# Optimization experiments

Hardware: AMD Instinct MI355X
Metric: run time of the kernel (lower is better)

## Reference

```python
import jax, jax.numpy as jnp
import numpy as np

B, S, T = 2, 4096, 4096
SRC, DST, WIDTH = 512, 512, 128
BLK = 128  # JAKAL_ADDITIVE_ROUTE_BLOCK_SIZE default


def setup_inputs() -> dict:
    key = jax.random.key(0)
    ks = jax.random.split(key, 7)
    return {
        "source_val": jax.random.normal(ks[0], (B, S, SRC), jnp.float32),
        "target_val": jax.random.normal(ks[1], (B, T, DST), jnp.float32),
        "Ws": jax.random.normal(ks[2], (WIDTH, SRC), jnp.float32) * 0.02,  # source_proj weight
        "Wt": jax.random.normal(ks[3], (WIDTH, DST), jnp.float32) * 0.02,  # target_proj weight
        "ws_out": jax.random.normal(ks[4], (WIDTH,), jnp.float32) * 0.02,  # source_out weight
        "wt_out": jax.random.normal(ks[5], (WIDTH,), jnp.float32) * 0.02,  # target_out weight
        "w_int": jax.random.normal(ks[6], (WIDTH,), jnp.float32) * 0.02,   # interaction_weight
        "bias": jnp.zeros((), jnp.float32),
    }


def reference(source_val, target_val, Ws, Wt, ws_out, wt_out, w_int, bias):
    # Projections (Linear without bias): y = x @ W.T
    ps = jnp.einsum('bsd,wd->bsw', source_val, Ws)   # [B,S,WIDTH]
    pt = jnp.einsum('btd,wd->btw', target_val, Wt)   # [B,T,WIDTH]
    s_lin = jnp.einsum('bsw,w->bs', ps, ws_out)      # [B,S]
    t_lin = jnp.einsum('btw,w->bt', pt, wt_out)      # [B,T]

    nblk = S // BLK
    # Block the source axis, matching the torch block loop (avoids a [B,S,T,W] tensor).
    ps_blocks = ps.reshape(B, nblk, BLK, WIDTH).transpose(1, 0, 2, 3)   # [nblk,B,BLK,W]
    sl_blocks = s_lin.reshape(B, nblk, BLK).transpose(1, 0, 2)          # [nblk,B,BLK]

    def block_scores(_, xs):
        ps_blk, sl_blk = xs
        # SiLU of the elementwise bilinear interaction, then low-rank weighted reduce.
        inter = jax.nn.silu(ps_blk[:, :, None, :] * pt[:, None, :, :])  # [B,BLK,T,W]
        sc = jnp.einsum('bktw,w->bkt', inter, w_int)
        sc = sc + sl_blk[:, :, None] + t_lin[:, None, :] + bias
        return None, sc

    _, out = jax.lax.scan(block_scores, None, (ps_blocks, sl_blocks))   # [nblk,B,BLK,T]
    return out.transpose(1, 0, 2, 3).reshape(B, S, T)
```

## Files before the change

kernel.cpp:

```cpp
#include <hip/hip_runtime.h>
#include <cstdint>
#include <cstddef>

#define B_ 2
#define S_ 4096
#define T_ 4096
#define D_ 512
#define W_ 128

#define A0C (-0.0006958f)
#define A1C (0.2529946f)
#define A2C (-0.0226345f)
#define A3C (0.0022173f)
#define A4C (-0.00011668f)
#define ZCUT 2.5f
#define ROWCAP 65536

typedef __attribute__((ext_vector_type(8))) short bf16x8;
typedef __attribute__((ext_vector_type(4))) float f32x4;

__device__ __forceinline__ uint16_t f2bf(float f){
  uint32_t u = __float_as_uint(f);
  u += 0x7FFFu + ((u >> 16) & 1u);
  return (uint16_t)(u >> 16);
}
__device__ __forceinline__ float bf2f(uint16_t h){
  return __uint_as_float(((uint32_t)h) << 16);
}

__device__ __forceinline__ void gl_lds16(const void* g, void* l){
  __builtin_amdgcn_global_load_lds(
      (const __attribute__((address_space(1))) void*)g,
      (__attribute__((address_space(3))) void*)l, 16, 0, 0);
}

union F4 { float4 v; float f[4]; };

template<int INBF>
__global__ void prep_k(const void* __restrict__ Ws, const void* __restrict__ Wt,
                       const void* __restrict__ wso, const void* __restrict__ wto,
                       const void* __restrict__ wi, const void* __restrict__ bias,
                       float* __restrict__ WsT, float* __restrict__ WtT,
                       float* __restrict__ wsof, float* __restrict__ wtof,
                       float* __restrict__ wif, float* __restrict__ cbias,
                       float* __restrict__ maxT, int* __restrict__ rowCnt){
  auto cv = [](const void* p, int i)->float{
    if (INBF) return bf2f(((const uint16_t*)p)[i]);
    return ((const float*)p)[i];
  };
  const void* in = (blockIdx.x & 1) ? Wt : Ws;
  float* out = (blockIdx.x & 1) ? WtT : WsT;
  int base = (blockIdx.x >> 1) * 4096;
  for (int o = base + threadIdx.x; o < base + 4096; o += blockDim.x){
    int d = o >> 7, w = o & (W_ - 1);
    out[o] = cv(in, w * D_ + d);
  }
  if (blockIdx.x == 1){
    maxT[threadIdx.x] = 0.f;
  }
  if (blockIdx.x == 0){
    if (threadIdx.x < W_){
      wsof[threadIdx.x] = cv(wso, threadIdx.x);
      wtof[threadIdx.x] = cv(wto, threadIdx.x);
      wif[threadIdx.x]  = cv(wi,  threadIdx.x);
    }
    __syncthreads();
    if (threadIdx.x == 0){
      float s = 0.f;
      for (int k = 0; k < W_; ++k) s += wif[k];
      cbias[0] = cv(bias, 0) + A0C * s;
      rowCnt[0] = 0;
    }
  }
}

template<int INBF, int MODE>
__global__ __launch_bounds__(256) void proj_k(const void* __restrict__ xraw,
        const float* __restrict__ WT, const float* __restrict__ wout,
        const float* __restrict__ wint,
        float* __restrict__ pT, float* __restrict__ lin,
        uint16_t* __restrict__ feat, float* __restrict__ maxT){
  __shared__ float xl[64 * 18];
  __shared__ float wl[64 * 128];
  int tid = threadIdx.x;
  int tx = tid & 31, ty = tid >> 5;
  int rowBase = blockIdx.x * 16;
  float acc[2][4] = {};
  for (int c = 0; c < 8; ++c){
    int d0 = c * 64;
    const float4* wt4 = (const float4*)(WT + (size_t)d0 * W_);
    float4* wl4 = (float4*)wl;
    #pragma unroll
    for (int p = 0; p < 8; ++p){ int q = tid + 256 * p; wl4[q] = wt4[q]; }
    {
      int q = tid;
      int r = q >> 4, dq = q & 15;
      float v0, v1, v2, v3;
      if (INBF){
        const uint16_t* xp = (const uint16_t*)xraw + (size_t)(rowBase + r) * D_ + d0 + dq * 4;
        ushort4 u = *(const ushort4*)xp;
        v0 = bf2f(u.x); v1 = bf2f(u.y); v2 = bf2f(u.z); v3 = bf2f(u.w);
      } else {
        const float* xp = (const float*)xraw + (size_t)(rowBase + r) * D_ + d0 + dq * 4;
        float4 u = *(const float4*)xp;
        v0 = u.x; v1 = u.y; v2 = u.z; v3 = u.w;
      }
      xl[(dq*4+0)*18 + r] = v0;
      xl[(dq*4+1)*18 + r] = v1;
      xl[(dq*4+2)*18 + r] = v2;
      xl[(dq*4+3)*18 + r] = v3;
    }
    __syncthreads();
    #pragma unroll 4
    for (int d = 0; d < 64; ++d){
      float a0 = xl[d * 18 + ty * 2 + 0];
      float a1 = xl[d * 18 + ty * 2 + 1];
      F4 w;
      w.v = *(const float4*)(wl + d * 128 + tx * 4);
      #pragma unroll
      for (int j = 0; j < 4; ++j){
        acc[0][j] = fmaf(a0, w.f[j], acc[0][j]);
        acc[1][j] = fmaf(a1, w.f[j], acc[1][j]);
      }
    }
    __syncthreads();
  }
  float* tile = wl;
  #pragma unroll
  for (int i = 0; i < 2; ++i)
    #pragma unroll
    for (int j = 0; j < 4; ++j)
      tile[(tx*4 + j) * 17 + ty*2 + i] = acc[i][j];
  F4 wo; wo.v = *(const float4*)(wout + tx * 4);
  F4 wiv;
  if (MODE == 0) wiv.v = *(const float4*)(wint + tx * 4);
  #pragma unroll
  for (int i = 0; i < 2; ++i){
    int r = rowBase + ty * 2 + i;
    float s = acc[i][0]*wo.f[0] + acc[i][1]*wo.f[1] + acc[i][2]*wo.f[2] + acc[i][3]*wo.f[3];
    #pragma unroll
    for (int off = 16; off >= 1; off >>= 1) s += __shfl_xor(s, off, 32);
    if (tx == 0) lin[r] = s;
    ushort4 g[5];
    uint16_t* gp = (uint16_t*)g;
    #pragma unroll
    for (int j = 0; j < 4; ++j){
      float p = acc[i][j];
      float p2 = p*p, p4 = p2*p2, p6 = p4*p2, p8 = p4*p4;
      float e0, e1, e2, e3, e4;
      if (MODE == 0){
        float wq = wiv.f[j];
        e0 = 0.5f * wq * p; e1 = A1C * wq * p2; e2 = A2C * wq * p4;
        e3 = A3C * wq * p6; e4 = A4C * wq * p8;
      } else {
        e0 = p; e1 = p2; e2 = p4; e3 = p6; e4 = p8;
      }
      gp[0*4+j] = f2bf(e0); gp[1*4+j] = f2bf(e1); gp[2*4+j] = f2bf(e2);
      gp[3*4+j] = f2bf(e3); gp[4*4+j] = f2bf(e4);
    }
    uint16_t* o = feat + (size_t)r * 640 + tx * 4;
    *(ushort4*)(o)       = g[0];
    *(ushort4*)(o + 128) = g[1];
    *(ushort4*)(o + 256) = g[2];
    *(ushort4*)(o + 384) = g[3];
    *(ushort4*)(o + 512) = g[4];
  }
  __syncthreads();
  int b = rowBase >> 12;
  {
    int w = tid >> 1, h = tid & 1;
    int sb = rowBase & (S_ - 1);
    float* dst = pT + ((size_t)(b * W_ + w)) * S_ + sb + h * 8;
    const float* src = tile + w * 17 + h * 8;
    #pragma unroll
    for (int k = 0; k < 2; ++k){
      float4 o = make_float4(src[k*4+0], src[k*4+1], src[k*4+2], src[k*4+3]);
      *(float4*)(dst + k * 4) = o;
    }
  }
  if (MODE == 1 && tid < W_){
    int w = tid;
    float m = 0.f;
    #pragma unroll
    for (int r = 0; r < 16; ++r) m = fmaxf(m, fabsf(tile[w * 17 + r]));
    atomicMax((unsigned int*)&maxT[b * W_ + w], __float_as_uint(m));
  }
}

template<int OUTBF>
__global__ __launch_bounds__(512) void gemm_k(const uint16_t* __restrict__ fA,
      const uint16_t* __restrict__ fB, const float* __restrict__ slin,
      const float* __restrict__ tlin, const float* __restrict__ cbias,
      void* __restrict__ outv){
  __shared__ __align__(16) uint16_t As[4][256 * 32];
  __shared__ __align__(16) uint16_t Bs[4][256 * 32];
  int tid = threadIdx.x, lane = tid & 63, wv = tid >> 6;
  int quad = lane >> 4, lr = lane & 15;
  int wm = wv >> 2, wn = wv & 3;
  int sl = quad ^ ((lane >> 1) & 3);
  int rowT = blockIdx.y * 256, colT = blockIdx.x * 256;
  int bb = rowT >> 12;

  const uint16_t* aBase = fA + (size_t)rowT * 640;
  const uint16_t* bBase = fB + ((size_t)bb * T_ + colT) * 640;

  int srw = tid >> 2;
  int k0 = (((tid & 3) ^ ((tid >> 3) & 3))) * 8;

  f32x4 acc[8][4];
  #pragma unroll
  for (int i = 0; i < 8; ++i)
    #pragma unroll
    for (int j = 0; j < 4; ++j)
      acc[i][j] = (f32x4){0.f, 0.f, 0.f, 0.f};

  auto STAGE = [&](int tile, int p){
    int sb = tile & 3;
    int kc = tile * 32;
    if (p == 0)
      gl_lds16(aBase + (size_t)srw * 640 + kc + k0,         &As[sb][tid * 8]);
    else if (p == 1)
      gl_lds16(aBase + (size_t)(128 + srw) * 640 + kc + k0, &As[sb][4096 + tid * 8]);
    else if (p == 2)
      gl_lds16(bBase + (size_t)srw * 640 + kc + k0,         &Bs[sb][tid * 8]);
    else
      gl_lds16(bBase + (size_t)(128 + srw) * 640 + kc + k0, &Bs[sb][4096 + tid * 8]);
  };

  #pragma unroll
  for (int p = 0; p < 4; ++p) STAGE(0, p);
  #pragma unroll
  for (int p = 0; p < 4; ++p) STAGE(1, p);
  asm volatile("s_waitcnt vmcnt(4)" ::: "memory");
  __builtin_amdgcn_s_barrier();

  for (int tile = 0; tile < 20; ++tile){
    int buf = tile & 3;
    bf16x8 bfr[4];
    #pragma unroll
    for (int p = 0; p < 4; ++p){
      bf16x8 a0 = *(const bf16x8*)&As[buf][(wm*128 + (2*p)*16   + lr) * 32 + sl * 8];
      bf16x8 a1 = *(const bf16x8*)&As[buf][(wm*128 + (2*p+1)*16 + lr) * 32 + sl * 8];
      if (p == 0){
        #pragma unroll
        for (int nj = 0; nj < 4; ++nj)
          bfr[nj] = *(const bf16x8*)&Bs[buf][(wn*64 + nj*16 + lr) * 32 + sl * 8];
      }
      if (tile + 2 < 20) STAGE(tile + 2, p);
      if (p == 3){
        if (tile + 2 < 20)   asm volatile("s_waitcnt vmcnt(4)" ::: "memory");
        else if (tile < 19)  asm volatile("s_waitcnt vmcnt(0)" ::: "memory");
      }
      __builtin_amdgcn_s_barrier();
      __builtin_amdgcn_s_setprio(1);
      #pragma unroll
      for (int nj = 0; nj < 4; ++nj){
        acc[2*p][nj]   = __builtin_amdgcn_mfma_f32_16x16x32_bf16(bfr[nj], a0, acc[2*p][nj],   0, 0, 0);
        acc[2*p+1][nj] = __builtin_amdgcn_mfma_f32_16x16x32_bf16(bfr[nj], a1, acc[2*p+1][nj], 0, 0, 0);
      }
      __builtin_amdgcn_s_setprio(0);
      __builtin_amdgcn_s_barrier();
    }
  }

  float cb = cbias[0];
  #pragma unroll
  for (int mi = 0; mi < 8; ++mi){
    int srow = rowT + wm * 128 + mi * 16 + lr;
    float sv = slin[srow] + cb;
    #pragma unroll
    for (int nj = 0; nj < 4; ++nj){
      int t0 = colT + wn * 64 + nj * 16 + quad * 4;
      F4 tl; tl.v = *(const float4*)(tlin + bb * T_ + t0);
      float o0 = acc[mi][nj][0] + sv + tl.f[0];
      float o1 = acc[mi][nj][1] + sv + tl.f[1];
      float o2 = acc[mi][nj][2] + sv + tl.f[2];
      float o3 = acc[mi][nj][3] + sv + tl.f[3];
      size_t oi = (size_t)srow * T_ + t0;
      if (OUTBF){
        ushort4 pk = make_ushort4(f2bf(o0), f2bf(o1), f2bf(o2), f2bf(o3));
        *(ushort4*)((uint16_t*)outv + oi) = pk;
      } else {
        *(float4*)((float*)outv + oi) = make_float4(o0, o1, o2, o3);
      }
    }
  }
}

__global__ void flagrows_k(const float* __restrict__ psT, const float* __restrict__ maxT,
                           uint32_t* __restrict__ rowList, int* __restrict__ rowCnt){
  int w = blockIdx.x, b = blockIdx.y;
  int tid = threadIdx.x;
  float mt = maxT[b * W_ + w];
  const float* psc = psT + (size_t)(b * W_ + w) * S_;
  for (int s = tid; s < S_; s += 256){
    float p = psc[s];
    if (fabsf(p) * mt > ZCUT){
      int k = atomicAdd(rowCnt, 1);
      if (k < ROWCAP)
        rowList[k] = ((uint32_t)b << 19) | ((uint32_t)w << 12) | (uint32_t)s;
    }
  }
}

template<int OUTBF>
__global__ __launch_bounds__(256) void fixscan_k(const float* __restrict__ psT,
        const float* __restrict__ ptT, const float* __restrict__ wint,
        const uint16_t* __restrict__ fA, const uint16_t* __restrict__ fB,
        const uint32_t* __restrict__ rowList, const int* __restrict__ rowCnt,
        void* __restrict__ outv){
  int n = *rowCnt; if (n > ROWCAP) n = ROWCAP;
  int tid = threadIdx.x;
  for (int job = blockIdx.x; job < n; job += gridDim.x){
    uint32_t pk = rowList[job];
    int b = (int)(pk >> 19), w = (int)((pk >> 12) & 127u), s = (int)(pk & 4095u);
    float wi = wint[w];
    float p = psT[(size_t)(b * W_ + w) * S_ + s];
    const float* ptc = ptT + (size_t)(b * W_ + w) * T_;
    const uint16_t* fa = fA + ((size_t)b * S_ + s) * 640 + w;
    float a0 = bf2f(fa[0]),   a1 = bf2f(fa[128]), a2 = bf2f(fa[256]);
    float a3 = bf2f(fa[384]), a4 = bf2f(fa[512]);
    for (int t = tid; t < T_; t += 256){
      float q = ptc[t];
      float z = p * q;
      if (fabsf(z) > ZCUT){
        const uint16_t* fb = fB + ((size_t)b * T_ + t) * 640 + w;
        float dot = a0 * bf2f(fb[0]) + a1 * bf2f(fb[128]) + a2 * bf2f(fb[256])
                  + a3 * bf2f(fb[384]) + a4 * bf2f(fb[512]);
        float sil = z / (1.0f + __expf(-z));
        float corr = wi * sil - dot - A0C * wi;
        size_t idx = ((size_t)b * S_ + s) * T_ + t;
        if (OUTBF){
          uint32_t* wp = (uint32_t*)outv + (idx >> 1);
          bool hi = (idx & 1u) != 0;
          uint32_t assumed, old = *wp;
          do {
            assumed = old;
            uint16_t h = hi ? (uint16_t)(assumed >> 16) : (uint16_t)(assumed & 0xFFFFu);
            uint16_t nh = f2bf(bf2f(h) + corr);
            uint32_t nw = hi ? ((assumed & 0x0000FFFFu) | ((uint32_t)nh << 16))
                             : ((assumed & 0xFFFF0000u) | (uint32_t)nh);
            old = atomicCAS(wp, assumed, nw);
          } while (old != assumed);
        } else {
          atomicAdd((float*)outv + idx, corr);
        }
      }
    }
  }
}

extern "C" void kernel_launch(void* const* d_in, const int* in_sizes, int n_in,
                              void* d_out, int out_size, void* d_ws, size_t ws_size,
                              hipStream_t stream){
  char* ws = (char*)d_ws;
  size_t off = 0;
  auto alloc = [&](size_t bytes)->char*{
    char* p = ws + off; off += (bytes + 255) & ~(size_t)255; return p;
  };
  float*    WsT  = (float*)   alloc((size_t)D_*W_*4);
  float*    WtT  = (float*)   alloc((size_t)D_*W_*4);
  float*    wsof = (float*)   alloc(W_*4);
  float*    wtof = (float*)   alloc(W_*4);
  float*    wif  = (float*)   alloc(W_*4);
  float*    cbias= (float*)   alloc(4);
  int*      rowCnt=(int*)     alloc(4);
  uint32_t* rowList=(uint32_t*)alloc((size_t)ROWCAP*4);
  float*    psT  = (float*)   alloc((size_t)B_*S_*W_*4);
  float*    ptT  = (float*)   alloc((size_t)B_*T_*W_*4);
  float*    slin = (float*)   alloc((size_t)B_*S_*4);
  float*    tlin = (float*)   alloc((size_t)B_*T_*4);
  float*    maxT = (float*)   alloc((size_t)B_*W_*4);
  uint16_t* featA= (uint16_t*)alloc((size_t)B_*S_*640*2);
  uint16_t* featB= (uint16_t*)alloc((size_t)B_*T_*640*2);

  bool inbf  = (in_sizes[0] == (int)((size_t)B_*S_*D_*2));
  bool outbf = (out_size    == (int)((size_t)B_*S_*T_*2));

  if (inbf){
    hipLaunchKernelGGL((prep_k<1>), dim3(32), dim3(256), 0, stream,
        d_in[2], d_in[3], d_in[4], d_in[5], d_in[6], d_in[7],
        WsT, WtT, wsof, wtof, wif, cbias, maxT, rowCnt);
    hipLaunchKernelGGL((proj_k<1,0>), dim3(B_*S_/16), dim3(256), 0, stream,
        d_in[0], WsT, wsof, wif, psT, slin, featA, maxT);
    hipLaunchKernelGGL((proj_k<1,1>), dim3(B_*T_/16), dim3(256), 0, stream,
        d_in[1], WtT, wtof, wif, ptT, tlin, featB, maxT);
  } else {
    hipLaunchKernelGGL((prep_k<0>), dim3(32), dim3(256), 0, stream,
        d_in[2], d_in[3], d_in[4], d_in[5], d_in[6], d_in[7],
        WsT, WtT, wsof, wtof, wif, cbias, maxT, rowCnt);
    hipLaunchKernelGGL((proj_k<0,0>), dim3(B_*S_/16), dim3(256), 0, stream,
        d_in[0], WsT, wsof, wif, psT, slin, featA, maxT);
    hipLaunchKernelGGL((proj_k<0,1>), dim3(B_*T_/16), dim3(256), 0, stream,
        d_in[1], WtT, wtof, wif, ptT, tlin, featB, maxT);
  }
  if (outbf)
    hipLaunchKernelGGL((gemm_k<1>), dim3(T_/256, B_*S_/256), dim3(512), 0, stream,
        featA, featB, slin, tlin, cbias, d_out);
  else
    hipLaunchKernelGGL((gemm_k<0>), dim3(T_/256, B_*S_/256), dim3(512), 0, stream,
        featA, featB, slin, tlin, cbias, d_out);
  hipLaunchKernelGGL(flagrows_k, dim3(W_, B_), dim3(256), 0, stream,
      psT, maxT, rowList, rowCnt);
  if (outbf)
    hipLaunchKernelGGL((fixscan_k<1>), dim3(2048), dim3(256), 0, stream,
        psT, ptT, wif, featA, featB, rowList, rowCnt, d_out);
  else
    hipLaunchKernelGGL((fixscan_k<0>), dim3(2048), dim3(256), 0, stream,
        psT, ptT, wif, featA, featB, rowList, rowCnt, d_out);
}
```

Before: 313.7 us.

## Simplify GEMM main loop to double-buffered LDS with one barrier pair per tile

```diff
diff --git a/kernel.cpp b/kernel.cpp
--- a/kernel.cpp
+++ b/kernel.cpp
@@ -192,8 +192,8 @@
       const uint16_t* __restrict__ fB, const float* __restrict__ slin,
       const float* __restrict__ tlin, const float* __restrict__ cbias,
       void* __restrict__ outv){
-  __shared__ __align__(16) uint16_t As[4][256 * 32];
-  __shared__ __align__(16) uint16_t Bs[4][256 * 32];
+  __shared__ __align__(16) uint16_t As[2][256 * 32];
+  __shared__ __align__(16) uint16_t Bs[2][256 * 32];
   int tid = threadIdx.x, lane = tid & 63, wv = tid >> 6;
   int quad = lane >> 4, lr = lane & 15;
   int wm = wv >> 2, wn = wv & 3;
@@ -214,53 +214,37 @@
     for (int j = 0; j < 4; ++j)
       acc[i][j] = (f32x4){0.f, 0.f, 0.f, 0.f};
 
-  auto STAGE = [&](int tile, int p){
-    int sb = tile & 3;
+  auto STAGE = [&](int tile){
+    int sb = tile & 1;
     int kc = tile * 32;
-    if (p == 0)
-      gl_lds16(aBase + (size_t)srw * 640 + kc + k0,         &As[sb][tid * 8]);
-    else if (p == 1)
-      gl_lds16(aBase + (size_t)(128 + srw) * 640 + kc + k0, &As[sb][4096 + tid * 8]);
-    else if (p == 2)
-      gl_lds16(bBase + (size_t)srw * 640 + kc + k0,         &Bs[sb][tid * 8]);
-    else
-      gl_lds16(bBase + (size_t)(128 + srw) * 640 + kc + k0, &Bs[sb][4096 + tid * 8]);
+    gl_lds16(aBase + (size_t)srw * 640 + kc + k0,         &As[sb][tid * 8]);
+    gl_lds16(aBase + (size_t)(128 + srw) * 640 + kc + k0, &As[sb][4096 + tid * 8]);
+    gl_lds16(bBase + (size_t)srw * 640 + kc + k0,         &Bs[sb][tid * 8]);
+    gl_lds16(bBase + (size_t)(128 + srw) * 640 + kc + k0, &Bs[sb][4096 + tid * 8]);
   };
 
-  #pragma unroll
-  for (int p = 0; p < 4; ++p) STAGE(0, p);
-  #pragma unroll
-  for (int p = 0; p < 4; ++p) STAGE(1, p);
-  asm volatile("s_waitcnt vmcnt(4)" ::: "memory");
-  __builtin_amdgcn_s_barrier();
-
+  STAGE(0);
   for (int tile = 0; tile < 20; ++tile){
-    int buf = tile & 3;
-    bf16x8 bfr[4];
-    #pragma unroll
-    for (int p = 0; p < 4; ++p){
-      bf16x8 a0 = *(const bf16x8*)&As[buf][(wm*128 + (2*p)*16   + lr) * 32 + sl * 8];
-      bf16x8 a1 = *(const bf16x8*)&As[buf][(wm*128 + (2*p+1)*16 + lr) * 32 + sl * 8];
-      if (p == 0){
-        #pragma unroll
-        for (int nj = 0; nj < 4; ++nj)
-          bfr[nj] = *(const bf16x8*)&Bs[buf][(wn*64 + nj*16 + lr) * 32 + sl * 8];
-      }
-      if (tile + 2 < 20) STAGE(tile + 2, p);
-      if (p == 3){
-        if (tile + 2 < 20)   asm volatile("s_waitcnt vmcnt(4)" ::: "memory");
-        else if (tile < 19)  asm volatile("s_waitcnt vmcnt(0)" ::: "memory");
-      }
-      __builtin_amdgcn_s_barrier();
-      __builtin_amdgcn_s_setprio(1);
+    int buf = tile & 1;
+    if (tile + 1 < 20){
+      STAGE(tile + 1);
+      asm volatile("s_waitcnt vmcnt(4)" ::: "memory");
+    } else {
+      asm volatile("s_waitcnt vmcnt(0)" ::: "memory");
+    }
+    __builtin_amdgcn_s_barrier();
+    bf16x8 bq[4];
+    #pragma unroll
+    for (int nj = 0; nj < 4; ++nj)
+      bq[nj] = *(const bf16x8*)&Bs[buf][(wn*64 + nj*16 + lr) * 32 + sl * 8];
+    #pragma unroll
+    for (int mi = 0; mi < 8; ++mi){
+      bf16x8 aq = *(const bf16x8*)&As[buf][(wm*128 + mi*16 + lr) * 32 + sl * 8];
       #pragma unroll
-      for (int nj = 0; nj < 4; ++nj){
-        acc[2*p][nj]   = __builtin_amdgcn_mfma_f32_16x16x32_bf16(bfr[nj], a0, acc[2*p][nj],   0, 0, 0);
-        acc[2*p+1][nj] = __builtin_amdgcn_mfma_f32_16x16x32_bf16(bfr[nj], a1, acc[2*p+1][nj], 0, 0, 0);
-      }
-      __builtin_amdgcn_s_setprio(0);
-      __builtin_amdgcn_s_barrier();
-    }
+      for (int nj = 0; nj < 4; ++nj)
+        acc[mi][nj] = __builtin_amdgcn_mfma_f32_16x16x32_bf16(bq[nj], aq, acc[mi][nj], 0, 0, 0);
+    }
+    __builtin_amdgcn_s_barrier();
   }
 
   float cb = cbias[0];
```

After: 308.4 us. No clear change (-1.7%).
